# Kernel optimization log

Measured on AMD Instinct MI355X. Metric: run time of the kernel, lower is better.

Reference implementation:

```python
import jax, jax.numpy as jnp
import numpy as np

B, N, E, C_IN, C_OUT, N_LAYERS = 4, 20000, 16, 128, 128, 3


def setup_inputs() -> dict:
    key = jax.random.key(0)
    kx, ke, k0, k1, k2 = jax.random.split(key, 5)
    x = jax.random.normal(kx, (B, N, C_IN), dtype=jnp.float32)
    # neighbor lists padded with -1 (as in the torch module)
    edge_index = jax.random.randint(ke, (B, N, E), -1, N, dtype=jnp.int32)
    s_in = 1.0 / np.sqrt(C_IN)
    s_out = 1.0 / np.sqrt(C_OUT)
    W0 = jax.random.uniform(k0, (C_OUT, C_IN), minval=-s_in, maxval=s_in, dtype=jnp.float32)
    W1 = jax.random.uniform(k1, (C_OUT, C_OUT), minval=-s_out, maxval=s_out, dtype=jnp.float32)
    W2 = jax.random.uniform(k2, (C_OUT, C_OUT), minval=-s_out, maxval=s_out, dtype=jnp.float32)
    return {"x": x, "edge_index": edge_index, "W0": W0, "W1": W1, "W2": W2}


def gcn_layer(x, edge_index, W):
    # x: [B, N, Cin], edge_index: [B, N, E] (pad = -1), W: [Cout, Cin]
    n_nodes = x.shape[1]
    deg = jnp.sum(edge_index >= 0, axis=-1, keepdims=True).astype(x.dtype) + 1.0  # [B,N,1]
    inv_sqrt_deg = 1.0 / jnp.sqrt(deg)
    h = jnp.einsum('bnc,oc->bno', x, W) * inv_sqrt_deg  # transform + 1/sqrt(deg)
    # padding row of zeros at index n_nodes; map -1 -> n_nodes
    padded = jnp.concatenate(
        [h, jnp.zeros((h.shape[0], 1, h.shape[2]), h.dtype)], axis=1)  # [B,N+1,Cout]
    idx = jnp.where(edge_index < 0, n_nodes, edge_index)
    neigh = jax.vmap(lambda p, e: p[e])(padded, idx)  # [B,N,E,Cout] gather
    # sum over neighbors + self, then scale again by 1/sqrt(deg)
    return (jnp.sum(neigh, axis=-2) + h) * inv_sqrt_deg


def reference(x, edge_index, W0, W1, W2):
    for W in (W0, W1, W2):
        x = jax.nn.elu(gcn_layer(x, edge_index, W))
    return x
```

## Files before the change

### kernel.cpp

```cpp
#include <hip/hip_runtime.h>

#define NB 4
#define NN 20000
#define NE 16
#define NC 128
#define M_TOTAL (NB * NN)

#define BM 64
#define BK 32
#define LDA (BM + 4)
#define LDW (NC + 4)

__global__ __launch_bounds__(256) void isd_kernel(const int* __restrict__ ei,
                                                  float* __restrict__ isd) {
    int g = blockIdx.x * 256 + threadIdx.x;
    if (g >= M_TOTAL) return;
    const int4* e4 = (const int4*)(ei + (size_t)g * NE);
    int cnt = 1;
#pragma unroll
    for (int q = 0; q < 4; ++q) {
        int4 v = e4[q];
        cnt += (v.x >= 0) + (v.y >= 0) + (v.z >= 0) + (v.w >= 0);
    }
    isd[g] = 1.0f / sqrtf((float)cnt);
}

__global__ __launch_bounds__(256, 4) void matmul_kernel(const float* __restrict__ X,
                                                        const float* __restrict__ W,
                                                        const float* __restrict__ isd,
                                                        float* __restrict__ H) {
    __shared__ float At[BK][LDA];
    __shared__ float Ws[BK][LDW];
    const int t = threadIdx.x;
    const int tx = t & 15;
    const int ty = t >> 4;
    const int bm = blockIdx.x * BM;

    float acc[4][8];
#pragma unroll
    for (int i = 0; i < 4; ++i)
#pragma unroll
        for (int j = 0; j < 8; ++j) acc[i][j] = 0.0f;

    for (int kk = 0; kk < NC; kk += BK) {
        __syncthreads();
        {
            const int m = t >> 2;
            const int c4 = (t & 3) << 3;
#pragma unroll
            for (int h = 0; h < 2; ++h) {
                const float4 v = *(const float4*)(X + (size_t)(bm + m) * NC + kk + c4 + h * 4);
                At[c4 + h * 4 + 0][m] = v.x;
                At[c4 + h * 4 + 1][m] = v.y;
                At[c4 + h * 4 + 2][m] = v.z;
                At[c4 + h * 4 + 3][m] = v.w;
            }
        }
        {
            const int o = t >> 1;
            const int c4 = (t & 1) << 4;
#pragma unroll
            for (int h = 0; h < 4; ++h) {
                const float4 v = *(const float4*)(W + (size_t)o * NC + kk + c4 + h * 4);
                Ws[c4 + h * 4 + 0][o] = v.x;
                Ws[c4 + h * 4 + 1][o] = v.y;
                Ws[c4 + h * 4 + 2][o] = v.z;
                Ws[c4 + h * 4 + 3][o] = v.w;
            }
        }
        __syncthreads();
#pragma unroll
        for (int kl = 0; kl < BK; ++kl) {
            const float4 a = *(const float4*)(&At[kl][ty << 2]);
            const float4 w0 = *(const float4*)(&Ws[kl][tx << 3]);
            const float4 w1 = *(const float4*)(&Ws[kl][(tx << 3) + 4]);
            const float av[4] = {a.x, a.y, a.z, a.w};
            const float wv[8] = {w0.x, w0.y, w0.z, w0.w, w1.x, w1.y, w1.z, w1.w};
#pragma unroll
            for (int i = 0; i < 4; ++i)
#pragma unroll
                for (int j = 0; j < 8; ++j)
                    acc[i][j] = fmaf(av[i], wv[j], acc[i][j]);
        }
    }

#pragma unroll
    for (int i = 0; i < 4; ++i) {
        const int m = bm + (ty << 2) + i;
        const float sd = isd[m];
        float4 o0, o1;
        o0.x = acc[i][0] * sd; o0.y = acc[i][1] * sd;
        o0.z = acc[i][2] * sd; o0.w = acc[i][3] * sd;
        o1.x = acc[i][4] * sd; o1.y = acc[i][5] * sd;
        o1.z = acc[i][6] * sd; o1.w = acc[i][7] * sd;
        *(float4*)(H + (size_t)m * NC + (tx << 3)) = o0;
        *(float4*)(H + (size_t)m * NC + (tx << 3) + 4) = o1;
    }
}

__global__ __launch_bounds__(256) void gather_kernel(const float* __restrict__ H,
                                                     const int* __restrict__ ei,
                                                     const float* __restrict__ isd,
                                                     float* __restrict__ out) {
    const int wid = threadIdx.x >> 6;
    const int lane = threadIdx.x & 63;
    int g = blockIdx.x * 4 + wid;
    g = __builtin_amdgcn_readfirstlane(g);
    const int base = (g / NN) * NN;

    const int4* e4 = (const int4*)(ei + (size_t)g * NE);
    const int4 ea = e4[0], eb = e4[1], ec = e4[2], ed = e4[3];
    const int e[NE] = {ea.x, ea.y, ea.z, ea.w, eb.x, eb.y, eb.z, eb.w,
                       ec.x, ec.y, ec.z, ec.w, ed.x, ed.y, ed.z, ed.w};

    const float2* h2 = (const float2*)H;
    float2 acc = h2[(size_t)g * 64 + lane];
#pragma unroll
    for (int q = 0; q < NE; ++q) {
        const int nbr = e[q];
        const int row = base + (nbr & ~(nbr >> 31));
        const float2 v = h2[(size_t)row * 64 + lane];
        if (nbr >= 0) { acc.x += v.x; acc.y += v.y; }
    }
    const float sd = isd[g];
    acc.x *= sd; acc.y *= sd;
    acc.x = acc.x > 0.0f ? acc.x : (__expf(acc.x) - 1.0f);
    acc.y = acc.y > 0.0f ? acc.y : (__expf(acc.y) - 1.0f);
    *(float2*)(out + (size_t)g * NC + (lane << 1)) = acc;
}

extern "C" void kernel_launch(void* const* d_in, const int* in_sizes, int n_in,
                              void* d_out, int out_size, void* d_ws, size_t ws_size,
                              hipStream_t stream) {
    const float* x = (const float*)d_in[0];
    const int* ei = (const int*)d_in[1];
    const float* W0 = (const float*)d_in[2];
    const float* W1 = (const float*)d_in[3];
    const float* W2 = (const float*)d_in[4];
    float* out = (float*)d_out;

    float* isd = (float*)d_ws;
    float* h = (float*)((char*)d_ws + (1 << 19));

    isd_kernel<<<(M_TOTAL + 255) / 256, 256, 0, stream>>>(ei, isd);

    matmul_kernel<<<M_TOTAL / BM, 256, 0, stream>>>(x, W0, isd, h);
    gather_kernel<<<M_TOTAL / 4, 256, 0, stream>>>(h, ei, isd, out);
    matmul_kernel<<<M_TOTAL / BM, 256, 0, stream>>>(out, W1, isd, h);
    gather_kernel<<<M_TOTAL / 4, 256, 0, stream>>>(h, ei, isd, out);
    matmul_kernel<<<M_TOTAL / BM, 256, 0, stream>>>(out, W2, isd, h);
    gather_kernel<<<M_TOTAL / 4, 256, 0, stream>>>(h, ei, isd, out);
}
```

Before: 433.8 us.

## Use split-bf16 MFMA matmul with prepacked weight fragments

```diff
diff --git a/kernel.cpp b/kernel.cpp
--- a/kernel.cpp
+++ b/kernel.cpp
@@ -1,15 +1,25 @@
 #include <hip/hip_runtime.h>
+#include <hip/hip_bf16.h>
 
 #define NB 4
 #define NN 20000
 #define NE 16
 #define NC 128
 #define M_TOTAL (NB * NN)
-
 #define BM 64
-#define BK 32
-#define LDA (BM + 4)
-#define LDW (NC + 4)
+
+typedef __attribute__((ext_vector_type(8))) short bf16x8;
+typedef __attribute__((ext_vector_type(4))) short short4v;
+typedef __attribute__((ext_vector_type(4))) float f32x4;
+
+static __device__ __forceinline__ short f2bf(float x) {
+    __hip_bfloat16 h = __float2bfloat16(x);
+    return *reinterpret_cast<short*>(&h);
+}
+static __device__ __forceinline__ float bf2f(short s) {
+    __hip_bfloat16 h = *reinterpret_cast<__hip_bfloat16*>(&s);
+    return __bfloat162float(h);
+}
 
 __global__ __launch_bounds__(256) void isd_kernel(const int* __restrict__ ei,
                                                   float* __restrict__ isd) {
@@ -25,77 +35,110 @@
     isd[g] = 1.0f / sqrtf((float)cnt);
 }
 
-__global__ __launch_bounds__(256, 4) void matmul_kernel(const float* __restrict__ X,
-                                                        const float* __restrict__ W,
-                                                        const float* __restrict__ isd,
-                                                        float* __restrict__ H) {
-    __shared__ float At[BK][LDA];
-    __shared__ float Ws[BK][LDW];
+__global__ __launch_bounds__(256) void wpack_kernel(const float* __restrict__ W,
+                                                    short* __restrict__ wp) {
+    const int id = blockIdx.x * 256 + threadIdx.x;
+    const int s = id >> 9;
+    const int f = (id >> 6) & 7;
+    const int l = id & 63;
+    const int o = f * 16 + (l & 15);
+    const int kb = s * 32 + (l >> 4) * 8;
+    const float4 v0 = *(const float4*)(W + (size_t)o * NC + kb);
+    const float4 v1 = *(const float4*)(W + (size_t)o * NC + kb + 4);
+    const float xs[8] = {v0.x, v0.y, v0.z, v0.w, v1.x, v1.y, v1.z, v1.w};
+    bf16x8 hv, lv;
+#pragma unroll
+    for (int e = 0; e < 8; ++e) {
+        const short h = f2bf(xs[e]);
+        hv[e] = h;
+        lv[e] = f2bf(xs[e] - bf2f(h));
+    }
+    short* dst = wp + (size_t)((s * 8 + f) * 2) * 512 + l * 8;
+    *(bf16x8*)dst = hv;
+    *(bf16x8*)(dst + 512) = lv;
+}
+
+__global__ __launch_bounds__(256) void matmul_kernel(const float* __restrict__ X,
+                                                     const short* __restrict__ wp,
+                                                     const float* __restrict__ isd,
+                                                     float* __restrict__ H) {
+    __shared__ short Ah[64 * 128];
+    __shared__ short Al[64 * 128];
     const int t = threadIdx.x;
-    const int tx = t & 15;
-    const int ty = t >> 4;
     const int bm = blockIdx.x * BM;
 
-    float acc[4][8];
-#pragma unroll
-    for (int i = 0; i < 4; ++i)
-#pragma unroll
-        for (int j = 0; j < 8; ++j) acc[i][j] = 0.0f;
-
-    for (int kk = 0; kk < NC; kk += BK) {
-        __syncthreads();
-        {
-            const int m = t >> 2;
-            const int c4 = (t & 3) << 3;
-#pragma unroll
-            for (int h = 0; h < 2; ++h) {
-                const float4 v = *(const float4*)(X + (size_t)(bm + m) * NC + kk + c4 + h * 4);
-                At[c4 + h * 4 + 0][m] = v.x;
-                At[c4 + h * 4 + 1][m] = v.y;
-                At[c4 + h * 4 + 2][m] = v.z;
-                At[c4 + h * 4 + 3][m] = v.w;
+#pragma unroll
+    for (int j = 0; j < 8; ++j) {
+        const int fi = j * 256 + t;
+        const int row = fi >> 5;
+        const int k0 = (t & 31) * 4;
+        const float4 v = *(const float4*)(X + (size_t)bm * NC + (size_t)fi * 4);
+        const float xs[4] = {v.x, v.y, v.z, v.w};
+        short4v hi, lo;
+#pragma unroll
+        for (int e = 0; e < 4; ++e) {
+            const short h = f2bf(xs[e]);
+            hi[e] = h;
+            lo[e] = f2bf(xs[e] - bf2f(h));
+        }
+        const int kblk = k0 >> 3;
+        const int dst = row * 128 + ((kblk ^ (row & 7)) << 3) + (k0 & 7);
+        *(short4v*)(Ah + dst) = hi;
+        *(short4v*)(Al + dst) = lo;
+    }
+    __syncthreads();
+
+    const int w = t >> 6, l = t & 63;
+    const int m0 = (w >> 1) * 32;
+    const int oh = w & 1;
+    const int lr = l & 15, lg = l >> 4;
+
+    f32x4 acc[2][4];
+#pragma unroll
+    for (int mf = 0; mf < 2; ++mf)
+#pragma unroll
+        for (int fi = 0; fi < 4; ++fi) acc[mf][fi] = (f32x4){0.f, 0.f, 0.f, 0.f};
+
+#pragma unroll
+    for (int s = 0; s < 4; ++s) {
+        bf16x8 a_h[2], a_l[2], b_h[4], b_l[4];
+#pragma unroll
+        for (int fi = 0; fi < 4; ++fi) {
+            const int fg = oh * 4 + fi;
+            const short* ph = wp + (size_t)((s * 8 + fg) * 2) * 512 + l * 8;
+            b_h[fi] = *(const bf16x8*)ph;
+            b_l[fi] = *(const bf16x8*)(ph + 512);
+        }
+#pragma unroll
+        for (int mf = 0; mf < 2; ++mf) {
+            const int row = m0 + mf * 16 + lr;
+            const int kblk = (s * 4 + lg) ^ (l & 7);
+            a_h[mf] = *(const bf16x8*)(Ah + row * 128 + kblk * 8);
+            a_l[mf] = *(const bf16x8*)(Al + row * 128 + kblk * 8);
+        }
+#pragma unroll
+        for (int mf = 0; mf < 2; ++mf)
+#pragma unroll
+            for (int fi = 0; fi < 4; ++fi) {
+                acc[mf][fi] = __builtin_amdgcn_mfma_f32_16x16x32_bf16(
+                    a_l[mf], b_h[fi], acc[mf][fi], 0, 0, 0);
+                acc[mf][fi] = __builtin_amdgcn_mfma_f32_16x16x32_bf16(
+                    a_h[mf], b_l[fi], acc[mf][fi], 0, 0, 0);
+                acc[mf][fi] = __builtin_amdgcn_mfma_f32_16x16x32_bf16(
+                    a_h[mf], b_h[fi], acc[mf][fi], 0, 0, 0);
             }
-        }
-        {
-            const int o = t >> 1;
-            const int c4 = (t & 1) << 4;
-#pragma unroll
-            for (int h = 0; h < 4; ++h) {
-                const float4 v = *(const float4*)(W + (size_t)o * NC + kk + c4 + h * 4);
-                Ws[c4 + h * 4 + 0][o] = v.x;
-                Ws[c4 + h * 4 + 1][o] = v.y;
-                Ws[c4 + h * 4 + 2][o] = v.z;
-                Ws[c4 + h * 4 + 3][o] = v.w;
-            }
-        }
-        __syncthreads();
-#pragma unroll
-        for (int kl = 0; kl < BK; ++kl) {
-            const float4 a = *(const float4*)(&At[kl][ty << 2]);
-            const float4 w0 = *(const float4*)(&Ws[kl][tx << 3]);
-            const float4 w1 = *(const float4*)(&Ws[kl][(tx << 3) + 4]);
-            const float av[4] = {a.x, a.y, a.z, a.w};
-            const float wv[8] = {w0.x, w0.y, w0.z, w0.w, w1.x, w1.y, w1.z, w1.w};
-#pragma unroll
-            for (int i = 0; i < 4; ++i)
-#pragma unroll
-                for (int j = 0; j < 8; ++j)
-                    acc[i][j] = fmaf(av[i], wv[j], acc[i][j]);
-        }
-    }
-
-#pragma unroll
-    for (int i = 0; i < 4; ++i) {
-        const int m = bm + (ty << 2) + i;
-        const float sd = isd[m];
-        float4 o0, o1;
-        o0.x = acc[i][0] * sd; o0.y = acc[i][1] * sd;
-        o0.z = acc[i][2] * sd; o0.w = acc[i][3] * sd;
-        o1.x = acc[i][4] * sd; o1.y = acc[i][5] * sd;
-        o1.z = acc[i][6] * sd; o1.w = acc[i][7] * sd;
-        *(float4*)(H + (size_t)m * NC + (tx << 3)) = o0;
-        *(float4*)(H + (size_t)m * NC + (tx << 3) + 4) = o1;
-    }
+    }
+
+#pragma unroll
+    for (int mf = 0; mf < 2; ++mf)
+#pragma unroll
+        for (int r = 0; r < 4; ++r) {
+            const int m = bm + m0 + mf * 16 + lg * 4 + r;
+            const float sd = isd[m];
+#pragma unroll
+            for (int fi = 0; fi < 4; ++fi)
+                H[(size_t)m * NC + oh * 64 + fi * 16 + lr] = acc[mf][fi][r] * sd;
+        }
 }
 
 __global__ __launch_bounds__(256) void gather_kernel(const float* __restrict__ H,
@@ -140,14 +183,20 @@
     float* out = (float*)d_out;
 
     float* isd = (float*)d_ws;
-    float* h = (float*)((char*)d_ws + (1 << 19));
+    short* wp0 = (short*)((char*)d_ws + (320 << 10));
+    short* wp1 = (short*)((char*)d_ws + (384 << 10));
+    short* wp2 = (short*)((char*)d_ws + (448 << 10));
+    float* h = (float*)((char*)d_ws + (512 << 10));
 
     isd_kernel<<<(M_TOTAL + 255) / 256, 256, 0, stream>>>(ei, isd);
-
-    matmul_kernel<<<M_TOTAL / BM, 256, 0, stream>>>(x, W0, isd, h);
+    wpack_kernel<<<8, 256, 0, stream>>>(W0, wp0);
+    wpack_kernel<<<8, 256, 0, stream>>>(W1, wp1);
+    wpack_kernel<<<8, 256, 0, stream>>>(W2, wp2);
+
+    matmul_kernel<<<M_TOTAL / BM, 256, 0, stream>>>(x, wp0, isd, h);
     gather_kernel<<<M_TOTAL / 4, 256, 0, stream>>>(h, ei, isd, out);
-    matmul_kernel<<<M_TOTAL / BM, 256, 0, stream>>>(out, W1, isd, h);
+    matmul_kernel<<<M_TOTAL / BM, 256, 0, stream>>>(out, wp1, isd, h);
     gather_kernel<<<M_TOTAL / 4, 256, 0, stream>>>(h, ei, isd, out);
-    matmul_kernel<<<M_TOTAL / BM, 256, 0, stream>>>(out, W2, isd, h);
+    matmul_kernel<<<M_TOTAL / BM, 256, 0, stream>>>(out, wp2, isd, h);
     gather_kernel<<<M_TOTAL / 4, 256, 0, stream>>>(h, ei, isd, out);
 }
```

New measurement: 378.2 us. -12.8%, faster.
